# Optimization experiments

Hardware: AMD Instinct MI355X
Metric: run time of the kernel (lower is better)

The kernel has to match this reference:

```python
import jax, jax.numpy as jnp
import numpy as np

N = 50000
E = 800000
NEG_SLOPE = 0.2
BN_EPS = 1e-5


def _gat_conv(x, src, dst, W, a_src, a_dst, bias, heads, out_ch, concat):
    # Linear projection per head: [N, heads, out_ch]
    h = (x @ W).reshape(-1, heads, out_ch)
    # Per-node attention terms alpha_src/alpha_dst: [N, heads]
    al_s = (h * a_src[None]).sum(-1)
    al_d = (h * a_dst[None]).sum(-1)
    # Edge logits with LeakyReLU: [E, heads]
    logits = jax.nn.leaky_relu(al_s[src] + al_d[dst], NEG_SLOPE)
    # Segment (scatter) softmax over edges grouped by destination node
    m = jax.ops.segment_max(logits, dst, num_segments=N)
    e = jnp.exp(logits - m[dst])
    s = jax.ops.segment_sum(e, dst, num_segments=N)
    alpha = e / (s[dst] + 1e-16)                      # [E, heads]
    # Weighted message aggregation: scatter-add to destinations
    msg = h[src] * alpha[:, :, None]                  # [E, heads, out_ch]
    out = jax.ops.segment_sum(msg, dst, num_segments=N)  # [N, heads, out_ch]
    out = out.reshape(-1, heads * out_ch) if concat else out.mean(axis=1)
    return out + bias


def _bn_eval(x, gamma, beta, mean, var):
    return (x - mean) * jax.lax.rsqrt(var + BN_EPS) * gamma + beta


def setup_inputs() -> dict:
    key = jax.random.key(0)
    ks = jax.random.split(key, 12)
    in_ch, hid, heads, out_cls = 128, 64, 2, 40
    return {
        "x": jax.random.normal(ks[0], (N, in_ch), jnp.float32),
        "edge_index": jax.random.randint(ks[1], (2, E), 0, N, jnp.int32),
        "W1": jax.random.normal(ks[2], (in_ch, heads * hid), jnp.float32) * 0.1,
        "a1_src": jax.random.normal(ks[3], (heads, hid), jnp.float32) * 0.1,
        "a1_dst": jax.random.normal(ks[4], (heads, hid), jnp.float32) * 0.1,
        "b1": jnp.zeros((heads * hid,), jnp.float32),
        "bn1_gamma": jnp.ones((heads * hid,), jnp.float32),
        "bn1_beta": jnp.zeros((heads * hid,), jnp.float32),
        "bn1_mean": jax.random.normal(ks[5], (heads * hid,), jnp.float32) * 0.1,
        "bn1_var": jax.random.uniform(ks[6], (heads * hid,), jnp.float32, 0.5, 1.5),
        "W2": jax.random.normal(ks[7], (heads * hid, out_cls), jnp.float32) * 0.1,
        "a2_src": jax.random.normal(ks[8], (1, out_cls), jnp.float32) * 0.1,
        "a2_dst": jax.random.normal(ks[9], (1, out_cls), jnp.float32) * 0.1,
        "b2": jnp.zeros((out_cls,), jnp.float32),
    }


def reference(x, edge_index, W1, a1_src, a1_dst, b1, bn1_gamma, bn1_beta,
              bn1_mean, bn1_var, W2, a2_src, a2_dst, b2):
    # add self loops
    loops = jnp.arange(N, dtype=edge_index.dtype)
    src = jnp.concatenate([edge_index[0], loops])
    dst = jnp.concatenate([edge_index[1], loops])
    # layer 1: GATConv(heads=2, concat) -> BN(eval) -> ReLU (dropout is eval no-op)
    h = _gat_conv(x, src, dst, W1, a1_src, a1_dst, b1, heads=2, out_ch=64, concat=True)
    h = jax.nn.relu(_bn_eval(h, bn1_gamma, bn1_beta, bn1_mean, bn1_var))
    # output layer: GATConv(heads=1, concat=False)
    out = _gat_conv(h, src, dst, W2, a2_src, a2_dst, b2, heads=1, out_ch=40, concat=False)
    return jax.nn.log_softmax(out, axis=1)
```

## Files before the change

kernel.cpp:

```cpp
#include <hip/hip_runtime.h>
#include <hip/hip_bf16.h>

#define NEG_SLOPE 0.2f
#define BN_EPS 1e-5f

#define NBLK 256
#define COARSE_SHIFT 9
#define COARSE_NPB 512

__device__ __forceinline__ float wred_sum(float v) {
    #pragma unroll
    for (int m = 32; m > 0; m >>= 1) v += __shfl_xor(v, m);
    return v;
}
__device__ __forceinline__ float wred_max(float v) {
    #pragma unroll
    for (int m = 32; m > 0; m >>= 1) v = fmaxf(v, __shfl_xor(v, m));
    return v;
}
__device__ __forceinline__ int wred_isum(int v) {
    #pragma unroll
    for (int m = 32; m > 0; m >>= 1) v += __shfl_xor(v, m);
    return v;
}
__device__ __forceinline__ float xor16_sum(float v) {
    #pragma unroll
    for (int m = 1; m < 16; m <<= 1) v += __shfl_xor(v, m);
    return v;
}

__device__ __forceinline__ unsigned pack_bf16(float a, float b) {
    __hip_bfloat162 t;
    t.x = __float2bfloat16(a);
    t.y = __float2bfloat16(b);
    return *(unsigned*)&t;
}
__device__ __forceinline__ float2 unpack_bf16(unsigned u) {
    __hip_bfloat162 t = *(__hip_bfloat162*)&u;
    return {__bfloat162float(t.x), __bfloat162float(t.y)};
}

__device__ __forceinline__ unsigned enc_ord(float f) {
    unsigned u = __float_as_uint(f);
    return (u & 0x80000000u) ? ~u : (u | 0x80000000u);
}
__device__ __forceinline__ float dec_ord(unsigned e) {
    unsigned u = (e & 0x80000000u) ? (e ^ 0x80000000u) : ~e;
    return __uint_as_float(u);
}

__global__ __launch_bounds__(256) void part_hist(const int* __restrict__ ei, int E, int Et,
                                                 int chunk, int* __restrict__ hist, int nCoarse) {
    __shared__ int h[128];
    int b = blockIdx.x, t = threadIdx.x;
    if (t < 128) h[t] = 0;
    __syncthreads();
    int beg = b * chunk, end = min(beg + chunk, Et);
    for (int idx = beg + t; idx < end; idx += 256) {
        int d = (idx < E) ? ei[E + idx] : (idx - E);
        atomicAdd(&h[d >> COARSE_SHIFT], 1);
    }
    __syncthreads();
    if (t < nCoarse) hist[t * NBLK + b] = h[t];
}

__global__ __launch_bounds__(1024) void csr_mid(int* __restrict__ hist,
                                                int* __restrict__ cbase, int nCoarse) {
    __shared__ int ctot_s[128];
    __shared__ int scn[128];
    __shared__ int cb_s[129];
    int t = threadIdx.x;
    int wv = t >> 6, ln = t & 63;
    if (t < 128) ctot_s[t] = 0;
    __syncthreads();
    for (int c = wv; c < nCoarse; c += 16) {
        int idx = c * NBLK + 4 * ln;
        int4 v = *(int4*)&hist[idx];
        int s = wred_isum(v.x + v.y + v.z + v.w);
        if (ln == 0) ctot_s[c] = s;
    }
    __syncthreads();
    int v0 = 0;
    if (t < 128) { v0 = ctot_s[t]; scn[t] = v0; }
    __syncthreads();
    for (int off = 1; off < 128; off <<= 1) {
        int u = (t >= off && t < 128) ? scn[t - off] : 0;
        __syncthreads();
        if (t < 128) scn[t] += u;
        __syncthreads();
    }
    if (t < 128) cb_s[t] = scn[t] - v0;
    if (t == 127) cb_s[128] = scn[127];
    __syncthreads();
    if (t <= nCoarse) cbase[t] = cb_s[t];
    for (int c = wv; c < nCoarse; c += 16) {
        int base = cb_s[c];
        int idx = c * NBLK + 4 * ln;
        int4 v = *(int4*)&hist[idx];
        int sl = v.x + v.y + v.z + v.w;
        int inc = sl;
        #pragma unroll
        for (int off = 1; off < 64; off <<= 1) {
            int u = __shfl_up(inc, off);
            if (ln >= off) inc += u;
        }
        int exc = inc - sl + base;
        int4 o;
        o.x = exc;
        o.y = exc + v.x;
        o.z = exc + v.x + v.y;
        o.w = exc + v.x + v.y + v.z;
        *(int4*)&hist[idx] = o;
    }
}

__global__ __launch_bounds__(256) void part_scatter(const int* __restrict__ ei, int E, int Et,
                                                    int chunk, const int* __restrict__ hist,
                                                    unsigned* __restrict__ staged, int nCoarse) {
    __shared__ int cur[128];
    int b = blockIdx.x, t = threadIdx.x;
    if (t < nCoarse) cur[t] = hist[t * NBLK + b];
    __syncthreads();
    int beg = b * chunk, end = min(beg + chunk, Et);
    for (int idx = beg + t; idx < end; idx += 256) {
        int s, d;
        if (idx < E) { s = ei[idx]; d = ei[E + idx]; }
        else         { s = idx - E; d = idx - E; }
        int c = d >> COARSE_SHIFT;
        int pos = atomicAdd(&cur[c], 1);
        staged[pos] = ((unsigned)s << COARSE_SHIFT) | (unsigned)(d & (COARSE_NPB - 1));
    }
}

__global__ __launch_bounds__(512) void fine_place(const unsigned* __restrict__ staged,
                                                  const int* __restrict__ cbase,
                                                  int* __restrict__ offs,
                                                  int* __restrict__ csr, int Nn, int nCoarse) {
    __shared__ int hcnt[COARSE_NPB];
    __shared__ int scn[COARSE_NPB];
    int b = blockIdx.x, t = threadIdx.x;
    int node0 = b << COARSE_SHIFT;
    int nloc = min(COARSE_NPB, Nn - node0);
    hcnt[t] = 0;
    __syncthreads();
    int ebeg = cbase[b], eend = cbase[b + 1];
    for (int p = ebeg + t; p < eend; p += 512) {
        atomicAdd(&hcnt[staged[p] & (COARSE_NPB - 1)], 1);
    }
    __syncthreads();
    int val = hcnt[t];
    scn[t] = val;
    __syncthreads();
    for (int off = 1; off < COARSE_NPB; off <<= 1) {
        int u = (t >= off) ? scn[t - off] : 0;
        __syncthreads();
        scn[t] += u;
        __syncthreads();
    }
    int exc = ebeg + scn[t] - val;
    if (t < nloc) offs[node0 + t] = exc;
    if (b == nCoarse - 1 && t == 0) offs[Nn] = eend;
    hcnt[t] = exc;
    __syncthreads();
    for (int p = ebeg + t; p < eend; p += 512) {
        unsigned v = staged[p];
        int pos = atomicAdd(&hcnt[v & (COARSE_NPB - 1)], 1);
        csr[pos] = (int)(v >> COARSE_SHIFT);
    }
}

__global__ __launch_bounds__(256) void gemm1_tiled(const float* __restrict__ x,
                                                   const float* __restrict__ W,
                                                   const float* __restrict__ a1s,
                                                   const float* __restrict__ a1d,
                                                   unsigned* __restrict__ h1b,
                                                   float* __restrict__ als,
                                                   float* __restrict__ ald, int Nn) {
    __shared__ float Ast[32][132];
    __shared__ float Bs[32][132];
    int t  = threadIdx.x;
    int tx = t & 15;
    int ty = t >> 4;
    int br = blockIdx.x * 128;

    float acc[8][8];
    #pragma unroll
    for (int i = 0; i < 8; ++i)
        #pragma unroll
        for (int j = 0; j < 8; ++j) acc[i][j] = 0.f;

    int k4   = t & 7;
    int rowA = t >> 3;

    for (int k0 = 0; k0 < 128; k0 += 32) {
        #pragma unroll
        for (int i = 0; i < 4; ++i) {
            int r  = rowA + 32 * i;
            int gr = min(br + r, Nn - 1);
            float4 v = *(const float4*)(x + (size_t)gr * 128 + k0 + 4 * k4);
            Ast[4 * k4 + 0][r] = v.x; Ast[4 * k4 + 1][r] = v.y;
            Ast[4 * k4 + 2][r] = v.z; Ast[4 * k4 + 3][r] = v.w;
        }
        #pragma unroll
        for (int i = 0; i < 4; ++i) {
            int f  = t + 256 * i;
            int kk = f >> 5, c4 = f & 31;
            *(float4*)&Bs[kk][4 * c4] = *(const float4*)(W + (size_t)(k0 + kk) * 128 + 4 * c4);
        }
        __syncthreads();
        #pragma unroll 8
        for (int kk = 0; kk < 32; ++kk) {
            float4 a0 = *(const float4*)&Ast[kk][8 * ty];
            float4 a1 = *(const float4*)&Ast[kk][8 * ty + 4];
            float4 b0 = *(const float4*)&Bs[kk][8 * tx];
            float4 b1 = *(const float4*)&Bs[kk][8 * tx + 4];
            float av[8] = {a0.x, a0.y, a0.z, a0.w, a1.x, a1.y, a1.z, a1.w};
            float bv[8] = {b0.x, b0.y, b0.z, b0.w, b1.x, b1.y, b1.z, b1.w};
            #pragma unroll
            for (int i = 0; i < 8; ++i)
                #pragma unroll
                for (int j = 0; j < 8; ++j) acc[i][j] += av[i] * bv[j];
        }
        __syncthreads();
    }

    float a_s[8], a_d[8];
    #pragma unroll
    for (int j = 0; j < 8; ++j) { a_s[j] = a1s[8 * tx + j]; a_d[j] = a1d[8 * tx + j]; }
    bool h0 = (tx < 8);

    #pragma unroll
    for (int i = 0; i < 8; ++i) {
        int r = br + 8 * ty + i;
        if (r < Nn) {
            uint4 pk;
            pk.x = pack_bf16(acc[i][0], acc[i][1]);
            pk.y = pack_bf16(acc[i][2], acc[i][3]);
            pk.z = pack_bf16(acc[i][4], acc[i][5]);
            pk.w = pack_bf16(acc[i][6], acc[i][7]);
            *(uint4*)(h1b + (size_t)r * 64 + 4 * tx) = pk;
        }
        float ps = 0.f, pd = 0.f;
        #pragma unroll
        for (int j = 0; j < 8; ++j) { ps += acc[i][j] * a_s[j]; pd += acc[i][j] * a_d[j]; }
        float s0 = xor16_sum(h0 ? ps : 0.f);
        float s1 = xor16_sum(h0 ? 0.f : ps);
        float d0 = xor16_sum(h0 ? pd : 0.f);
        float d1 = xor16_sum(h0 ? 0.f : pd);
        if (tx == 0 && r < Nn) {
            als[r * 2] = s0; als[r * 2 + 1] = s1;
            ald[r * 2] = d0; ald[r * 2 + 1] = d1;
        }
    }
}

template <int H>
__global__ __launch_bounds__(256) void almax_kernel(const float* __restrict__ als,
                                                    unsigned* __restrict__ gmax, int off, int Nn,
                                                    const float* __restrict__ b1,
                                                    const float* __restrict__ g1,
                                                    const float* __restrict__ be1,
                                                    const float* __restrict__ mn1,
                                                    const float* __restrict__ vr1,
                                                    float* __restrict__ bnscale,
                                                    float* __restrict__ bnshift) {
    __shared__ float red[4][H];
    int t = threadIdx.x;
    if (bnscale && blockIdx.x == 0 && t < 128) {
        float sc = rsqrtf(vr1[t] + BN_EPS) * g1[t];
        bnscale[t] = sc;
        bnshift[t] = be1[t] + (b1[t] - mn1[t]) * sc;
    }
    float m[H];
    #pragma unroll
    for (int h = 0; h < H; ++h) m[h] = -1e30f;
    for (int n = blockIdx.x * 256 + t; n < Nn; n += gridDim.x * 256) {
        #pragma unroll
        for (int h = 0; h < H; ++h) m[h] = fmaxf(m[h], als[n * H + h]);
    }
    #pragma unroll
    for (int h = 0; h < H; ++h) m[h] = wred_max(m[h]);
    int wid = t >> 6;
    if ((t & 63) == 0) {
        #pragma unroll
        for (int h = 0; h < H; ++h) red[wid][h] = m[h];
    }
    __syncthreads();
    if (t == 0) {
        #pragma unroll
        for (int h = 0; h < H; ++h) {
            float mm = fmaxf(fmaxf(red[0][h], red[1][h]), fmaxf(red[2][h], red[3][h]));
            atomicMax(&gmax[off + h], enc_ord(mm));
        }
    }
}

__global__ __launch_bounds__(256) void softagg1_kernel(const int* __restrict__ offs, const int* __restrict__ csr,
                            const unsigned* __restrict__ h1b,
                            const float* __restrict__ als, const float* __restrict__ ald,
                            const unsigned* __restrict__ gmax,
                            const float* __restrict__ bnscale, const float* __restrict__ bnshift,
                            unsigned* __restrict__ hbnb, int Nn) {
    __shared__ int   sh_s[4][64];
    __shared__ float sh_e0[4][64];
    __shared__ float sh_e1[4][64];
    int wid = threadIdx.x >> 6, lane = threadIdx.x & 63;
    int n = blockIdx.x * 4 + wid;
    if (n >= Nn) return;
    int b = offs[n], e = offs[n + 1];
    float2 aldn = *(const float2*)(ald + n * 2);
    float bd0 = dec_ord(gmax[0]) + aldn.x; bd0 = (bd0 > 0.f) ? bd0 : NEG_SLOPE * bd0;
    float bd1 = dec_ord(gmax[1]) + aldn.y; bd1 = (bd1 > 0.f) ? bd1 : NEG_SLOPE * bd1;

    int eslot = lane >> 3;
    int l8    = lane & 7;
    float acc[16];
    #pragma unroll
    for (int j = 0; j < 16; ++j) acc[j] = 0.f;
    float den0 = 0.f, den1 = 0.f;

    for (int base = b; base < e; base += 64) {
        int cnt = min(64, e - base);
        int   s1 = 0;
        float e0r = 0.f, e1r = 0.f;
        if (lane < cnt) {
            s1 = csr[base + lane];
            float2 as = *(const float2*)(als + (size_t)s1 * 2);
            float l0 = as.x + aldn.x; l0 = (l0 > 0.f) ? l0 : NEG_SLOPE * l0;
            float l1 = as.y + aldn.y; l1 = (l1 > 0.f) ? l1 : NEG_SLOPE * l1;
            e0r = __expf(l0 - bd0);
            e1r = __expf(l1 - bd1);
            den0 += e0r; den1 += e1r;
        }
        sh_s[wid][lane]  = s1;
        sh_e0[wid][lane] = e0r;
        sh_e1[wid][lane] = e1r;
        int i = eslot;
        for (; i + 8 < cnt; i += 16) {
            int   sA  = sh_s[wid][i];
            int   sB  = sh_s[wid][i + 8];
            float e0A = sh_e0[wid][i],  e1A = sh_e1[wid][i];
            float e0B = sh_e0[wid][i + 8], e1B = sh_e1[wid][i + 8];
            const uint4* pA = (const uint4*)(h1b + (size_t)sA * 64 + 4 * l8);
            const uint4* pB = (const uint4*)(h1b + (size_t)sB * 64 + 4 * l8);
            uint4 vaA = pA[0];
            uint4 vbA = pA[8];
            uint4 vaB = pB[0];
            uint4 vbB = pB[8];
            float2 f;
            f = unpack_bf16(vaA.x); acc[0]  += f.x * e0A; acc[1]  += f.y * e0A;
            f = unpack_bf16(vaA.y); acc[2]  += f.x * e0A; acc[3]  += f.y * e0A;
            f = unpack_bf16(vaA.z); acc[4]  += f.x * e0A; acc[5]  += f.y * e0A;
            f = unpack_bf16(vaA.w); acc[6]  += f.x * e0A; acc[7]  += f.y * e0A;
            f = unpack_bf16(vbA.x); acc[8]  += f.x * e1A; acc[9]  += f.y * e1A;
            f = unpack_bf16(vbA.y); acc[10] += f.x * e1A; acc[11] += f.y * e1A;
            f = unpack_bf16(vbA.z); acc[12] += f.x * e1A; acc[13] += f.y * e1A;
            f = unpack_bf16(vbA.w); acc[14] += f.x * e1A; acc[15] += f.y * e1A;
            f = unpack_bf16(vaB.x); acc[0]  += f.x * e0B; acc[1]  += f.y * e0B;
            f = unpack_bf16(vaB.y); acc[2]  += f.x * e0B; acc[3]  += f.y * e0B;
            f = unpack_bf16(vaB.z); acc[4]  += f.x * e0B; acc[5]  += f.y * e0B;
            f = unpack_bf16(vaB.w); acc[6]  += f.x * e0B; acc[7]  += f.y * e0B;
            f = unpack_bf16(vbB.x); acc[8]  += f.x * e1B; acc[9]  += f.y * e1B;
            f = unpack_bf16(vbB.y); acc[10] += f.x * e1B; acc[11] += f.y * e1B;
            f = unpack_bf16(vbB.z); acc[12] += f.x * e1B; acc[13] += f.y * e1B;
            f = unpack_bf16(vbB.w); acc[14] += f.x * e1B; acc[15] += f.y * e1B;
        }
        if (i < cnt) {
            int   s  = sh_s[wid][i];
            float e0 = sh_e0[wid][i], e1 = sh_e1[wid][i];
            const uint4* pR = (const uint4*)(h1b + (size_t)s * 64 + 4 * l8);
            uint4 va = pR[0];
            uint4 vb = pR[8];
            float2 f;
            f = unpack_bf16(va.x); acc[0]  += f.x * e0; acc[1]  += f.y * e0;
            f = unpack_bf16(va.y); acc[2]  += f.x * e0; acc[3]  += f.y * e0;
            f = unpack_bf16(va.z); acc[4]  += f.x * e0; acc[5]  += f.y * e0;
            f = unpack_bf16(va.w); acc[6]  += f.x * e0; acc[7]  += f.y * e0;
            f = unpack_bf16(vb.x); acc[8]  += f.x * e1; acc[9]  += f.y * e1;
            f = unpack_bf16(vb.y); acc[10] += f.x * e1; acc[11] += f.y * e1;
            f = unpack_bf16(vb.z); acc[12] += f.x * e1; acc[13] += f.y * e1;
            f = unpack_bf16(vb.w); acc[14] += f.x * e1; acc[15] += f.y * e1;
        }
    }
    #pragma unroll
    for (int j = 0; j < 16; ++j) {
        acc[j] += __shfl_xor(acc[j], 8);
        acc[j] += __shfl_xor(acc[j], 16);
        acc[j] += __shfl_xor(acc[j], 32);
    }
    den0 = wred_sum(den0);
    den1 = wred_sum(den1);
    if (eslot == 0) {
        float inv0 = 1.f / (den0 + 1e-16f);
        float inv1 = 1.f / (den1 + 1e-16f);
        int c0 = 8 * l8, c1 = 64 + 8 * l8;
        float4 sa = *(const float4*)(bnscale + c0), sb = *(const float4*)(bnscale + c0 + 4);
        float4 ha = *(const float4*)(bnshift + c0), hb = *(const float4*)(bnshift + c0 + 4);
        float o0 = fmaxf(acc[0] * inv0 * sa.x + ha.x, 0.f);
        float o1 = fmaxf(acc[1] * inv0 * sa.y + ha.y, 0.f);
        float o2 = fmaxf(acc[2] * inv0 * sa.z + ha.z, 0.f);
        float o3 = fmaxf(acc[3] * inv0 * sa.w + ha.w, 0.f);
        float o4 = fmaxf(acc[4] * inv0 * sb.x + hb.x, 0.f);
        float o5 = fmaxf(acc[5] * inv0 * sb.y + hb.y, 0.f);
        float o6 = fmaxf(acc[6] * inv0 * sb.z + hb.z, 0.f);
        float o7 = fmaxf(acc[7] * inv0 * sb.w + hb.w, 0.f);
        uint4 pk0 = {pack_bf16(o0, o1), pack_bf16(o2, o3), pack_bf16(o4, o5), pack_bf16(o6, o7)};
        *(uint4*)(hbnb + (size_t)n * 64 + 4 * l8) = pk0;
        float4 sc = *(const float4*)(bnscale + c1), sd = *(const float4*)(bnscale + c1 + 4);
        float4 hc = *(const float4*)(bnshift + c1), hd = *(const float4*)(bnshift + c1 + 4);
        float p0 = fmaxf(acc[8]  * inv1 * sc.x + hc.x, 0.f);
        float p1 = fmaxf(acc[9]  * inv1 * sc.y + hc.y, 0.f);
        float p2 = fmaxf(acc[10] * inv1 * sc.z + hc.z, 0.f);
        float p3 = fmaxf(acc[11] * inv1 * sc.w + hc.w, 0.f);
        float p4 = fmaxf(acc[12] * inv1 * sd.x + hd.x, 0.f);
        float p5 = fmaxf(acc[13] * inv1 * sd.y + hd.y, 0.f);
        float p6 = fmaxf(acc[14] * inv1 * sd.z + hd.z, 0.f);
        float p7 = fmaxf(acc[15] * inv1 * sd.w + hd.w, 0.f);
        uint4 pk1 = {pack_bf16(p0, p1), pack_bf16(p2, p3), pack_bf16(p4, p5), pack_bf16(p6, p7)};
        *(uint4*)(hbnb + (size_t)n * 64 + 32 + 4 * l8) = pk1;
    }
}

__global__ __launch_bounds__(256) void gemm2_tiled(const unsigned* __restrict__ hbnb,
                                                   const float* __restrict__ W2,
                                                   const float* __restrict__ a2s,
                                                   const float* __restrict__ a2d,
                                                   unsigned* __restrict__ h2b,
                                                   float* __restrict__ als, float* __restrict__ ald,
                                                   int Nn) {
    __shared__ float Ast[32][132];
    __shared__ float Bs[32][68];
    int t  = threadIdx.x;
    int tx = t & 15;
    int ty = t >> 4;
    int br = blockIdx.x * 128;

    float as4[4], ad4[4];
    #pragma unroll
    for (int j = 0; j < 4; ++j) {
        int c = 4 * tx + j;
        as4[j] = (c < 40) ? a2s[c] : 0.f;
        ad4[j] = (c < 40) ? a2d[c] : 0.f;
    }

    float acc[8][4];
    #pragma unroll
    for (int i = 0; i < 8; ++i)
        #pragma unroll
        for (int j = 0; j < 4; ++j) acc[i][j] = 0.f;

    int k4   = t & 7;
    int rowA = t >> 3;

    for (int k0 = 0; k0 < 128; k0 += 32) {
        #pragma unroll
        for (int i = 0; i < 4; ++i) {
            int r  = rowA + 32 * i;
            int gr = min(br + r, Nn - 1);
            uint2 v2 = *(const uint2*)(hbnb + (size_t)gr * 64 + (k0 >> 1) + 2 * k4);
            float2 f0 = unpack_bf16(v2.x), f1 = unpack_bf16(v2.y);
            Ast[4 * k4 + 0][r] = f0.x; Ast[4 * k4 + 1][r] = f0.y;
            Ast[4 * k4 + 2][r] = f1.x; Ast[4 * k4 + 3][r] = f1.y;
        }
        #pragma unroll
        for (int i = 0; i < 2; ++i) {
            int f  = t + 256 * i;
            int kk = f >> 4, c4 = f & 15;
            float4 v = {0.f, 0.f, 0.f, 0.f};
            if (c4 < 10) v = *(const float4*)(W2 + (size_t)(k0 + kk) * 40 + 4 * c4);
            *(float4*)&Bs[kk][4 * c4] = v;
        }
        __syncthreads();
        #pragma unroll 8
        for (int kk = 0; kk < 32; ++kk) {
            float4 a0 = *(const float4*)&Ast[kk][8 * ty];
            float4 a1 = *(const float4*)&Ast[kk][8 * ty + 4];
            float4 b0 = *(const float4*)&Bs[kk][4 * tx];
            float av[8] = {a0.x, a0.y, a0.z, a0.w, a1.x, a1.y, a1.z, a1.w};
            #pragma unroll
            for (int i = 0; i < 8; ++i) {
                acc[i][0] += av[i] * b0.x; acc[i][1] += av[i] * b0.y;
                acc[i][2] += av[i] * b0.z; acc[i][3] += av[i] * b0.w;
            }
        }
        __syncthreads();
    }

    #pragma unroll
    for (int i = 0; i < 8; ++i) {
        int r = br + 8 * ty + i;
        if (r < Nn) {
            uint2 pk = {pack_bf16(acc[i][0], acc[i][1]), pack_bf16(acc[i][2], acc[i][3])};
            *(uint2*)(h2b + (size_t)r * 32 + 2 * tx) = pk;
        }
        float ps = acc[i][0] * as4[0] + acc[i][1] * as4[1] + acc[i][2] * as4[2] + acc[i][3] * as4[3];
        float pd = acc[i][0] * ad4[0] + acc[i][1] * ad4[1] + acc[i][2] * ad4[2] + acc[i][3] * ad4[3];
        float sS = xor16_sum(ps);
        float sD = xor16_sum(pd);
        if (tx == 0 && r < Nn) { als[r] = sS; ald[r] = sD; }
    }
}

__global__ __launch_bounds__(256) void softagg2_kernel(const int* __restrict__ offs, const int* __restrict__ csr,
                            const unsigned* __restrict__ h2b,
                            const float* __restrict__ als, const float* __restrict__ ald,
                            const unsigned* __restrict__ gmax,
                            const float* __restrict__ b2,
                            float* __restrict__ out, int Nn) {
    __shared__ int   sh_s[4][64];
    __shared__ float sh_ev[4][64];
    int wid = threadIdx.x >> 6, lane = threadIdx.x & 63;
    int n = blockIdx.x * 4 + wid;
    if (n >= Nn) return;
    int b = offs[n], e = offs[n + 1];
    float aldn = ald[n];
    float bound = dec_ord(gmax[2]) + aldn;
    bound = (bound > 0.f) ? bound : NEG_SLOPE * bound;

    int eslot = lane >> 3;
    int l8    = lane & 7;
    float acc[8];
    #pragma unroll
    for (int j = 0; j < 8; ++j) acc[j] = 0.f;
    float den = 0.f;

    for (int base = b; base < e; base += 64) {
        int cnt = min(64, e - base);
        int   s1 = 0;
        float evr = 0.f;
        if (lane < cnt) {
            s1 = csr[base + lane];
            float l = als[s1] + aldn;
            l = (l > 0.f) ? l : NEG_SLOPE * l;
            evr = __expf(l - bound);
            den += evr;
        }
        sh_s[wid][lane]  = s1;
        sh_ev[wid][lane] = evr;
        int i = eslot;
        for (; i + 8 < cnt; i += 16) {
            int   sA  = sh_s[wid][i];
            int   sB  = sh_s[wid][i + 8];
            float evA = sh_ev[wid][i];
            float evB = sh_ev[wid][i + 8];
            uint4 vA = *(const uint4*)(h2b + (size_t)sA * 32 + 4 * l8);
            uint4 vB = *(const uint4*)(h2b + (size_t)sB * 32 + 4 * l8);
            float2 f;
            f = unpack_bf16(vA.x); acc[0] += f.x * evA; acc[1] += f.y * evA;
            f = unpack_bf16(vA.y); acc[2] += f.x * evA; acc[3] += f.y * evA;
            f = unpack_bf16(vA.z); acc[4] += f.x * evA; acc[5] += f.y * evA;
            f = unpack_bf16(vA.w); acc[6] += f.x * evA; acc[7] += f.y * evA;
            f = unpack_bf16(vB.x); acc[0] += f.x * evB; acc[1] += f.y * evB;
            f = unpack_bf16(vB.y); acc[2] += f.x * evB; acc[3] += f.y * evB;
            f = unpack_bf16(vB.z); acc[4] += f.x * evB; acc[5] += f.y * evB;
            f = unpack_bf16(vB.w); acc[6] += f.x * evB; acc[7] += f.y * evB;
        }
        if (i < cnt) {
            int   s  = sh_s[wid][i];
            float ev = sh_ev[wid][i];
            uint4 v = *(const uint4*)(h2b + (size_t)s * 32 + 4 * l8);
            float2 f;
            f = unpack_bf16(v.x); acc[0] += f.x * ev; acc[1] += f.y * ev;
            f = unpack_bf16(v.y); acc[2] += f.x * ev; acc[3] += f.y * ev;
            f = unpack_bf16(v.z); acc[4] += f.x * ev; acc[5] += f.y * ev;
            f = unpack_bf16(v.w); acc[6] += f.x * ev; acc[7] += f.y * ev;
        }
    }
    #pragma unroll
    for (int j = 0; j < 8; ++j) {
        acc[j] += __shfl_xor(acc[j], 8);
        acc[j] += __shfl_xor(acc[j], 16);
        acc[j] += __shfl_xor(acc[j], 32);
    }
    den = wred_sum(den);
    float inv = 1.f / (den + 1e-16f);
    bool valid = (eslot == 0) && (l8 < 5);
    float vv[8];
    float lmax = -1e30f;
    if (valid) {
        int c = 8 * l8;
        #pragma unroll
        for (int j = 0; j < 8; ++j) {
            vv[j] = acc[j] * inv + b2[c + j];
            lmax = fmaxf(lmax, vv[j]);
        }
    }
    float m = wred_max(lmax);
    float es = 0.f;
    if (valid) {
        #pragma unroll
        for (int j = 0; j < 8; ++j) es += __expf(vv[j] - m);
    }
    float ssum = wred_sum(es);
    float lse = m + logf(ssum);
    if (valid) {
        float4 oa = {vv[0] - lse, vv[1] - lse, vv[2] - lse, vv[3] - lse};
        float4 ob = {vv[4] - lse, vv[5] - lse, vv[6] - lse, vv[7] - lse};
        *(float4*)(out + (size_t)n * 40 + 8 * l8)     = oa;
        *(float4*)(out + (size_t)n * 40 + 8 * l8 + 4) = ob;
    }
}

extern "C" void kernel_launch(void* const* d_in, const int* in_sizes, int n_in,
                              void* d_out, int out_size, void* d_ws, size_t ws_size,
                              hipStream_t stream) {
    const float* x    = (const float*)d_in[0];
    const int*   ei   = (const int*)d_in[1];
    const float* W1   = (const float*)d_in[2];
    const float* a1s  = (const float*)d_in[3];
    const float* a1d  = (const float*)d_in[4];
    const float* b1   = (const float*)d_in[5];
    const float* g1   = (const float*)d_in[6];
    const float* be1  = (const float*)d_in[7];
    const float* mn1  = (const float*)d_in[8];
    const float* vr1  = (const float*)d_in[9];
    const float* W2   = (const float*)d_in[10];
    const float* a2s  = (const float*)d_in[11];
    const float* a2d  = (const float*)d_in[12];
    const float* b2   = (const float*)d_in[13];
    float* out = (float*)d_out;

    const int N  = in_sizes[0] / 128;
    const int E  = in_sizes[1] / 2;
    const int Et = E + N;
    const int nCoarse = (N + COARSE_NPB - 1) >> COARSE_SHIFT;
    const int chunk   = (Et + NBLK - 1) / NBLK;

    char* p = (char*)d_ws;
    auto alloc = [&](size_t bytes) -> void* {
        void* r = (void*)p;
        p += (bytes + 255) & ~(size_t)255;
        return r;
    };
    int*      hist   = (int*)alloc((size_t)nCoarse * NBLK * 4);
    int*      cbase  = (int*)alloc((size_t)(nCoarse + 1) * 4);
    int*      offs   = (int*)alloc((size_t)(N + 1) * 4);
    unsigned* staged = (unsigned*)alloc((size_t)Et * 4);
    int*      csr    = (int*)alloc((size_t)Et * 4);
    unsigned* h1b    = (unsigned*)alloc((size_t)N * 64 * 4);
    float*    al1sv  = (float*)alloc((size_t)N * 2 * 4);
    float*    al1dv  = (float*)alloc((size_t)N * 2 * 4);
    unsigned* hbnb   = (unsigned*)alloc((size_t)N * 64 * 4);
    unsigned* h2b    = (unsigned*)alloc((size_t)N * 32 * 4);
    float*    al2sv  = (float*)alloc((size_t)N * 4);
    float*    al2dv  = (float*)alloc((size_t)N * 4);
    unsigned* gmax   = (unsigned*)alloc(4 * 4);
    float*    bnscale= (float*)alloc(128 * 4);
    float*    bnshift= (float*)alloc(128 * 4);
    (void)ws_size;

    hipMemsetAsync(gmax, 0, 16, stream);

    part_hist<<<NBLK, 256, 0, stream>>>(ei, E, Et, chunk, hist, nCoarse);
    csr_mid<<<1, 1024, 0, stream>>>(hist, cbase, nCoarse);
    part_scatter<<<NBLK, 256, 0, stream>>>(ei, E, Et, chunk, hist, staged, nCoarse);
    fine_place<<<nCoarse, 512, 0, stream>>>(staged, cbase, offs, csr, N, nCoarse);

    gemm1_tiled<<<(N + 127) / 128, 256, 0, stream>>>(x, W1, a1s, a1d, h1b, al1sv, al1dv, N);
    almax_kernel<2><<<64, 256, 0, stream>>>(al1sv, gmax, 0, N, b1, g1, be1, mn1, vr1, bnscale, bnshift);
    softagg1_kernel<<<(N + 3) / 4, 256, 0, stream>>>(offs, csr, h1b, al1sv, al1dv, gmax,
                                                     bnscale, bnshift, hbnb, N);

    gemm2_tiled<<<(N + 127) / 128, 256, 0, stream>>>(hbnb, W2, a2s, a2d, h2b, al2sv, al2dv, N);
    almax_kernel<1><<<64, 256, 0, stream>>>(al2sv, gmax, 2, N, nullptr, nullptr, nullptr, nullptr,
                                            nullptr, nullptr, nullptr);
    softagg2_kernel<<<(N + 3) / 4, 256, 0, stream>>>(offs, csr, h2b, al2sv, al2dv, gmax, b2, out, N);
}
```

Before: 264.9 us.

## Map multiple destination nodes per wavefront and compact layer-2 feature rows

Both aggregation kernels now assign a sub-group of lanes (16 for layer 1, 8 for layer 2) to each destination node instead of a whole 64-lane wavefront. This removes the cross-slot shuffle reductions and the idle lanes caused by the low average degree (about 17). The layer-2 bf16 feature buffer is shrunk from a 32-word row stride to 20 words, which cuts gather bytes. In exchange each lane walks edges serially, so latency for high-degree nodes grows, and there is less memory-level parallelism per node.

Result: faster. 241.3 us (-8.9%).

```diff
diff --git a/kernel.cpp b/kernel.cpp
--- a/kernel.cpp
+++ b/kernel.cpp
@@ -301,30 +301,30 @@
                             const unsigned* __restrict__ gmax,
                             const float* __restrict__ bnscale, const float* __restrict__ bnshift,
                             unsigned* __restrict__ hbnb, int Nn) {
-    __shared__ int   sh_s[4][64];
-    __shared__ float sh_e0[4][64];
-    __shared__ float sh_e1[4][64];
+    __shared__ int   sh_s[4][4][16];
+    __shared__ float sh_e[4][4][2][16];
     int wid = threadIdx.x >> 6, lane = threadIdx.x & 63;
-    int n = blockIdx.x * 4 + wid;
+    int g = lane >> 4;
+    int l = lane & 15;
+    int head = l >> 3;
+    int n = blockIdx.x * 16 + wid * 4 + g;
     if (n >= Nn) return;
     int b = offs[n], e = offs[n + 1];
-    float2 aldn = *(const float2*)(ald + n * 2);
+    float2 aldn = *(const float2*)(ald + (size_t)n * 2);
     float bd0 = dec_ord(gmax[0]) + aldn.x; bd0 = (bd0 > 0.f) ? bd0 : NEG_SLOPE * bd0;
     float bd1 = dec_ord(gmax[1]) + aldn.y; bd1 = (bd1 > 0.f) ? bd1 : NEG_SLOPE * bd1;
 
-    int eslot = lane >> 3;
-    int l8    = lane & 7;
-    float acc[16];
-    #pragma unroll
-    for (int j = 0; j < 16; ++j) acc[j] = 0.f;
+    float acc[8];
+    #pragma unroll
+    for (int j = 0; j < 8; ++j) acc[j] = 0.f;
     float den0 = 0.f, den1 = 0.f;
 
-    for (int base = b; base < e; base += 64) {
-        int cnt = min(64, e - base);
+    for (int base = b; base < e; base += 16) {
+        int cnt = min(16, e - base);
         int   s1 = 0;
         float e0r = 0.f, e1r = 0.f;
-        if (lane < cnt) {
-            s1 = csr[base + lane];
+        if (l < cnt) {
+            s1 = csr[base + l];
             float2 as = *(const float2*)(als + (size_t)s1 * 2);
             float l0 = as.x + aldn.x; l0 = (l0 > 0.f) ? l0 : NEG_SLOPE * l0;
             float l1 = as.y + aldn.y; l1 = (l1 > 0.f) ? l1 : NEG_SLOPE * l1;
@@ -332,93 +332,57 @@
             e1r = __expf(l1 - bd1);
             den0 += e0r; den1 += e1r;
         }
-        sh_s[wid][lane]  = s1;
-        sh_e0[wid][lane] = e0r;
-        sh_e1[wid][lane] = e1r;
-        int i = eslot;
-        for (; i + 8 < cnt; i += 16) {
-            int   sA  = sh_s[wid][i];
-            int   sB  = sh_s[wid][i + 8];
-            float e0A = sh_e0[wid][i],  e1A = sh_e1[wid][i];
-            float e0B = sh_e0[wid][i + 8], e1B = sh_e1[wid][i + 8];
-            const uint4* pA = (const uint4*)(h1b + (size_t)sA * 64 + 4 * l8);
-            const uint4* pB = (const uint4*)(h1b + (size_t)sB * 64 + 4 * l8);
-            uint4 vaA = pA[0];
-            uint4 vbA = pA[8];
-            uint4 vaB = pB[0];
-            uint4 vbB = pB[8];
+        sh_s[wid][g][l]    = s1;
+        sh_e[wid][g][0][l] = e0r;
+        sh_e[wid][g][1][l] = e1r;
+        int i = 0;
+        for (; i + 1 < cnt; i += 2) {
+            int   sA  = sh_s[wid][g][i];
+            int   sB  = sh_s[wid][g][i + 1];
+            float evA = sh_e[wid][g][head][i];
+            float evB = sh_e[wid][g][head][i + 1];
+            uint4 vA = *(const uint4*)(h1b + (size_t)sA * 64 + 4 * l);
+            uint4 vB = *(const uint4*)(h1b + (size_t)sB * 64 + 4 * l);
             float2 f;
-            f = unpack_bf16(vaA.x); acc[0]  += f.x * e0A; acc[1]  += f.y * e0A;
-            f = unpack_bf16(vaA.y); acc[2]  += f.x * e0A; acc[3]  += f.y * e0A;
-            f = unpack_bf16(vaA.z); acc[4]  += f.x * e0A; acc[5]  += f.y * e0A;
-            f = unpack_bf16(vaA.w); acc[6]  += f.x * e0A; acc[7]  += f.y * e0A;
-            f = unpack_bf16(vbA.x); acc[8]  += f.x * e1A; acc[9]  += f.y * e1A;
-            f = unpack_bf16(vbA.y); acc[10] += f.x * e1A; acc[11] += f.y * e1A;
-            f = unpack_bf16(vbA.z); acc[12] += f.x * e1A; acc[13] += f.y * e1A;
-            f = unpack_bf16(vbA.w); acc[14] += f.x * e1A; acc[15] += f.y * e1A;
-            f = unpack_bf16(vaB.x); acc[0]  += f.x * e0B; acc[1]  += f.y * e0B;
-            f = unpack_bf16(vaB.y); acc[2]  += f.x * e0B; acc[3]  += f.y * e0B;
-            f = unpack_bf16(vaB.z); acc[4]  += f.x * e0B; acc[5]  += f.y * e0B;
-            f = unpack_bf16(vaB.w); acc[6]  += f.x * e0B; acc[7]  += f.y * e0B;
-            f = unpack_bf16(vbB.x); acc[8]  += f.x * e1B; acc[9]  += f.y * e1B;
-            f = unpack_bf16(vbB.y); acc[10] += f.x * e1B; acc[11] += f.y * e1B;
-            f = unpack_bf16(vbB.z); acc[12] += f.x * e1B; acc[13] += f.y * e1B;
-            f = unpack_bf16(vbB.w); acc[14] += f.x * e1B; acc[15] += f.y * e1B;
+            f = unpack_bf16(vA.x); acc[0] += f.x * evA; acc[1] += f.y * evA;
+            f = unpack_bf16(vA.y); acc[2] += f.x * evA; acc[3] += f.y * evA;
+            f = unpack_bf16(vA.z); acc[4] += f.x * evA; acc[5] += f.y * evA;
+            f = unpack_bf16(vA.w); acc[6] += f.x * evA; acc[7] += f.y * evA;
+            f = unpack_bf16(vB.x); acc[0] += f.x * evB; acc[1] += f.y * evB;
+            f = unpack_bf16(vB.y); acc[2] += f.x * evB; acc[3] += f.y * evB;
+            f = unpack_bf16(vB.z); acc[4] += f.x * evB; acc[5] += f.y * evB;
+            f = unpack_bf16(vB.w); acc[6] += f.x * evB; acc[7] += f.y * evB;
         }
         if (i < cnt) {
-            int   s  = sh_s[wid][i];
-            float e0 = sh_e0[wid][i], e1 = sh_e1[wid][i];
-            const uint4* pR = (const uint4*)(h1b + (size_t)s * 64 + 4 * l8);
-            uint4 va = pR[0];
-            uint4 vb = pR[8];
+            int   s  = sh_s[wid][g][i];
+            float ev = sh_e[wid][g][head][i];
+            uint4 v = *(const uint4*)(h1b + (size_t)s * 64 + 4 * l);
             float2 f;
-            f = unpack_bf16(va.x); acc[0]  += f.x * e0; acc[1]  += f.y * e0;
-            f = unpack_bf16(va.y); acc[2]  += f.x * e0; acc[3]  += f.y * e0;
-            f = unpack_bf16(va.z); acc[4]  += f.x * e0; acc[5]  += f.y * e0;
-            f = unpack_bf16(va.w); acc[6]  += f.x * e0; acc[7]  += f.y * e0;
-            f = unpack_bf16(vb.x); acc[8]  += f.x * e1; acc[9]  += f.y * e1;
-            f = unpack_bf16(vb.y); acc[10] += f.x * e1; acc[11] += f.y * e1;
-            f = unpack_bf16(vb.z); acc[12] += f.x * e1; acc[13] += f.y * e1;
-            f = unpack_bf16(vb.w); acc[14] += f.x * e1; acc[15] += f.y * e1;
-        }
-    }
-    #pragma unroll
-    for (int j = 0; j < 16; ++j) {
-        acc[j] += __shfl_xor(acc[j], 8);
-        acc[j] += __shfl_xor(acc[j], 16);
-        acc[j] += __shfl_xor(acc[j], 32);
-    }
-    den0 = wred_sum(den0);
-    den1 = wred_sum(den1);
-    if (eslot == 0) {
-        float inv0 = 1.f / (den0 + 1e-16f);
-        float inv1 = 1.f / (den1 + 1e-16f);
-        int c0 = 8 * l8, c1 = 64 + 8 * l8;
-        float4 sa = *(const float4*)(bnscale + c0), sb = *(const float4*)(bnscale + c0 + 4);
-        float4 ha = *(const float4*)(bnshift + c0), hb = *(const float4*)(bnshift + c0 + 4);
-        float o0 = fmaxf(acc[0] * inv0 * sa.x + ha.x, 0.f);
-        float o1 = fmaxf(acc[1] * inv0 * sa.y + ha.y, 0.f);
-        float o2 = fmaxf(acc[2] * inv0 * sa.z + ha.z, 0.f);
-        float o3 = fmaxf(acc[3] * inv0 * sa.w + ha.w, 0.f);
-        float o4 = fmaxf(acc[4] * inv0 * sb.x + hb.x, 0.f);
-        float o5 = fmaxf(acc[5] * inv0 * sb.y + hb.y, 0.f);
-        float o6 = fmaxf(acc[6] * inv0 * sb.z + hb.z, 0.f);
-        float o7 = fmaxf(acc[7] * inv0 * sb.w + hb.w, 0.f);
-        uint4 pk0 = {pack_bf16(o0, o1), pack_bf16(o2, o3), pack_bf16(o4, o5), pack_bf16(o6, o7)};
-        *(uint4*)(hbnb + (size_t)n * 64 + 4 * l8) = pk0;
-        float4 sc = *(const float4*)(bnscale + c1), sd = *(const float4*)(bnscale + c1 + 4);
-        float4 hc = *(const float4*)(bnshift + c1), hd = *(const float4*)(bnshift + c1 + 4);
-        float p0 = fmaxf(acc[8]  * inv1 * sc.x + hc.x, 0.f);
-        float p1 = fmaxf(acc[9]  * inv1 * sc.y + hc.y, 0.f);
-        float p2 = fmaxf(acc[10] * inv1 * sc.z + hc.z, 0.f);
-        float p3 = fmaxf(acc[11] * inv1 * sc.w + hc.w, 0.f);
-        float p4 = fmaxf(acc[12] * inv1 * sd.x + hd.x, 0.f);
-        float p5 = fmaxf(acc[13] * inv1 * sd.y + hd.y, 0.f);
-        float p6 = fmaxf(acc[14] * inv1 * sd.z + hd.z, 0.f);
-        float p7 = fmaxf(acc[15] * inv1 * sd.w + hd.w, 0.f);
-        uint4 pk1 = {pack_bf16(p0, p1), pack_bf16(p2, p3), pack_bf16(p4, p5), pack_bf16(p6, p7)};
-        *(uint4*)(hbnb + (size_t)n * 64 + 32 + 4 * l8) = pk1;
-    }
+            f = unpack_bf16(v.x); acc[0] += f.x * ev; acc[1] += f.y * ev;
+            f = unpack_bf16(v.y); acc[2] += f.x * ev; acc[3] += f.y * ev;
+            f = unpack_bf16(v.z); acc[4] += f.x * ev; acc[5] += f.y * ev;
+            f = unpack_bf16(v.w); acc[6] += f.x * ev; acc[7] += f.y * ev;
+        }
+    }
+    #pragma unroll
+    for (int m = 1; m < 16; m <<= 1) {
+        den0 += __shfl_xor(den0, m);
+        den1 += __shfl_xor(den1, m);
+    }
+    float inv = 1.f / ((head ? den1 : den0) + 1e-16f);
+    int c = 8 * l;
+    float4 sa = *(const float4*)(bnscale + c), sb = *(const float4*)(bnscale + c + 4);
+    float4 ha = *(const float4*)(bnshift + c), hb = *(const float4*)(bnshift + c + 4);
+    float o0 = fmaxf(acc[0] * inv * sa.x + ha.x, 0.f);
+    float o1 = fmaxf(acc[1] * inv * sa.y + ha.y, 0.f);
+    float o2 = fmaxf(acc[2] * inv * sa.z + ha.z, 0.f);
+    float o3 = fmaxf(acc[3] * inv * sa.w + ha.w, 0.f);
+    float o4 = fmaxf(acc[4] * inv * sb.x + hb.x, 0.f);
+    float o5 = fmaxf(acc[5] * inv * sb.y + hb.y, 0.f);
+    float o6 = fmaxf(acc[6] * inv * sb.z + hb.z, 0.f);
+    float o7 = fmaxf(acc[7] * inv * sb.w + hb.w, 0.f);
+    uint4 pk = {pack_bf16(o0, o1), pack_bf16(o2, o3), pack_bf16(o4, o5), pack_bf16(o6, o7)};
+    *(uint4*)(hbnb + (size_t)n * 64 + 4 * l) = pk;
 }
 
 __global__ __launch_bounds__(256) void gemm2_tiled(const unsigned* __restrict__ hbnb,
@@ -489,9 +453,9 @@
     #pragma unroll
     for (int i = 0; i < 8; ++i) {
         int r = br + 8 * ty + i;
-        if (r < Nn) {
+        if (r < Nn && tx < 10) {
             uint2 pk = {pack_bf16(acc[i][0], acc[i][1]), pack_bf16(acc[i][2], acc[i][3])};
-            *(uint2*)(h2b + (size_t)r * 32 + 2 * tx) = pk;
+            *(uint2*)(h2b + (size_t)r * 20 + 2 * tx) = pk;
         }
         float ps = acc[i][0] * as4[0] + acc[i][1] * as4[1] + acc[i][2] * as4[2] + acc[i][3] * as4[3];
         float pd = acc[i][0] * ad4[0] + acc[i][1] * ad4[1] + acc[i][2] * ad4[2] + acc[i][3] * ad4[3];
@@ -507,97 +471,97 @@
                             const unsigned* __restrict__ gmax,
                             const float* __restrict__ b2,
                             float* __restrict__ out, int Nn) {
-    __shared__ int   sh_s[4][64];
-    __shared__ float sh_ev[4][64];
+    __shared__ int   sh_s[4][8][8];
+    __shared__ float sh_ev[4][8][8];
     int wid = threadIdx.x >> 6, lane = threadIdx.x & 63;
-    int n = blockIdx.x * 4 + wid;
+    int g = lane >> 3;
+    int l = lane & 7;
+    int n = blockIdx.x * 32 + wid * 8 + g;
     if (n >= Nn) return;
     int b = offs[n], e = offs[n + 1];
     float aldn = ald[n];
     float bound = dec_ord(gmax[2]) + aldn;
     bound = (bound > 0.f) ? bound : NEG_SLOPE * bound;
 
-    int eslot = lane >> 3;
-    int l8    = lane & 7;
     float acc[8];
     #pragma unroll
     for (int j = 0; j < 8; ++j) acc[j] = 0.f;
     float den = 0.f;
 
-    for (int base = b; base < e; base += 64) {
-        int cnt = min(64, e - base);
+    for (int base = b; base < e; base += 8) {
+        int cnt = min(8, e - base);
         int   s1 = 0;
         float evr = 0.f;
-        if (lane < cnt) {
-            s1 = csr[base + lane];
-            float l = als[s1] + aldn;
-            l = (l > 0.f) ? l : NEG_SLOPE * l;
-            evr = __expf(l - bound);
+        if (l < cnt) {
+            s1 = csr[base + l];
+            float lv = als[s1] + aldn;
+            lv = (lv > 0.f) ? lv : NEG_SLOPE * lv;
+            evr = __expf(lv - bound);
             den += evr;
         }
-        sh_s[wid][lane]  = s1;
-        sh_ev[wid][lane] = evr;
-        int i = eslot;
-        for (; i + 8 < cnt; i += 16) {
-            int   sA  = sh_s[wid][i];
-            int   sB  = sh_s[wid][i + 8];
-            float evA = sh_ev[wid][i];
-            float evB = sh_ev[wid][i + 8];
-            uint4 vA = *(const uint4*)(h2b + (size_t)sA * 32 + 4 * l8);
-            uint4 vB = *(const uint4*)(h2b + (size_t)sB * 32 + 4 * l8);
-            float2 f;
-            f = unpack_bf16(vA.x); acc[0] += f.x * evA; acc[1] += f.y * evA;
-            f = unpack_bf16(vA.y); acc[2] += f.x * evA; acc[3] += f.y * evA;
-            f = unpack_bf16(vA.z); acc[4] += f.x * evA; acc[5] += f.y * evA;
-            f = unpack_bf16(vA.w); acc[6] += f.x * evA; acc[7] += f.y * evA;
-            f = unpack_bf16(vB.x); acc[0] += f.x * evB; acc[1] += f.y * evB;
-            f = unpack_bf16(vB.y); acc[2] += f.x * evB; acc[3] += f.y * evB;
-            f = unpack_bf16(vB.z); acc[4] += f.x * evB; acc[5] += f.y * evB;
-            f = unpack_bf16(vB.w); acc[6] += f.x * evB; acc[7] += f.y * evB;
-        }
-        if (i < cnt) {
-            int   s  = sh_s[wid][i];
-            float ev = sh_ev[wid][i];
-            uint4 v = *(const uint4*)(h2b + (size_t)s * 32 + 4 * l8);
-            float2 f;
-            f = unpack_bf16(v.x); acc[0] += f.x * ev; acc[1] += f.y * ev;
-            f = unpack_bf16(v.y); acc[2] += f.x * ev; acc[3] += f.y * ev;
-            f = unpack_bf16(v.z); acc[4] += f.x * ev; acc[5] += f.y * ev;
-            f = unpack_bf16(v.w); acc[6] += f.x * ev; acc[7] += f.y * ev;
-        }
-    }
-    #pragma unroll
-    for (int j = 0; j < 8; ++j) {
-        acc[j] += __shfl_xor(acc[j], 8);
-        acc[j] += __shfl_xor(acc[j], 16);
-        acc[j] += __shfl_xor(acc[j], 32);
-    }
-    den = wred_sum(den);
+        sh_s[wid][g][l]  = s1;
+        sh_ev[wid][g][l] = evr;
+        if (l < 5) {
+            int i = 0;
+            for (; i + 1 < cnt; i += 2) {
+                int   sA  = sh_s[wid][g][i];
+                int   sB  = sh_s[wid][g][i + 1];
+                float evA = sh_ev[wid][g][i];
+                float evB = sh_ev[wid][g][i + 1];
+                uint4 vA = *(const uint4*)(h2b + (size_t)sA * 20 + 4 * l);
+                uint4 vB = *(const uint4*)(h2b + (size_t)sB * 20 + 4 * l);
+                float2 f;
+                f = unpack_bf16(vA.x); acc[0] += f.x * evA; acc[1] += f.y * evA;
+                f = unpack_bf16(vA.y); acc[2] += f.x * evA; acc[3] += f.y * evA;
+                f = unpack_bf16(vA.z); acc[4] += f.x * evA; acc[5] += f.y * evA;
+                f = unpack_bf16(vA.w); acc[6] += f.x * evA; acc[7] += f.y * evA;
+                f = unpack_bf16(vB.x); acc[0] += f.x * evB; acc[1] += f.y * evB;
+                f = unpack_bf16(vB.y); acc[2] += f.x * evB; acc[3] += f.y * evB;
+                f = unpack_bf16(vB.z); acc[4] += f.x * evB; acc[5] += f.y * evB;
+                f = unpack_bf16(vB.w); acc[6] += f.x * evB; acc[7] += f.y * evB;
+            }
+            if (i < cnt) {
+                int   s  = sh_s[wid][g][i];
+                float ev = sh_ev[wid][g][i];
+                uint4 v = *(const uint4*)(h2b + (size_t)s * 20 + 4 * l);
+                float2 f;
+                f = unpack_bf16(v.x); acc[0] += f.x * ev; acc[1] += f.y * ev;
+                f = unpack_bf16(v.y); acc[2] += f.x * ev; acc[3] += f.y * ev;
+                f = unpack_bf16(v.z); acc[4] += f.x * ev; acc[5] += f.y * ev;
+                f = unpack_bf16(v.w); acc[6] += f.x * ev; acc[7] += f.y * ev;
+            }
+        }
+    }
+    #pragma unroll
+    for (int m = 1; m < 8; m <<= 1) den += __shfl_xor(den, m);
     float inv = 1.f / (den + 1e-16f);
-    bool valid = (eslot == 0) && (l8 < 5);
+    bool valid = (l < 5);
     float vv[8];
     float lmax = -1e30f;
     if (valid) {
-        int c = 8 * l8;
+        int c = 8 * l;
         #pragma unroll
         for (int j = 0; j < 8; ++j) {
             vv[j] = acc[j] * inv + b2[c + j];
             lmax = fmaxf(lmax, vv[j]);
         }
     }
-    float m = wred_max(lmax);
+    float m = lmax;
+    #pragma unroll
+    for (int mm = 1; mm < 8; mm <<= 1) m = fmaxf(m, __shfl_xor(m, mm));
     float es = 0.f;
     if (valid) {
         #pragma unroll
         for (int j = 0; j < 8; ++j) es += __expf(vv[j] - m);
     }
-    float ssum = wred_sum(es);
-    float lse = m + logf(ssum);
+    #pragma unroll
+    for (int mm = 1; mm < 8; mm <<= 1) es += __shfl_xor(es, mm);
+    float lse = m + logf(es);
     if (valid) {
         float4 oa = {vv[0] - lse, vv[1] - lse, vv[2] - lse, vv[3] - lse};
         float4 ob = {vv[4] - lse, vv[5] - lse, vv[6] - lse, vv[7] - lse};
-        *(float4*)(out + (size_t)n * 40 + 8 * l8)     = oa;
-        *(float4*)(out + (size_t)n * 40 + 8 * l8 + 4) = ob;
+        *(float4*)(out + (size_t)n * 40 + 8 * l)     = oa;
+        *(float4*)(out + (size_t)n * 40 + 8 * l + 4) = ob;
     }
 }
 
@@ -641,7 +605,7 @@
     float*    al1sv  = (float*)alloc((size_t)N * 2 * 4);
     float*    al1dv  = (float*)alloc((size_t)N * 2 * 4);
     unsigned* hbnb   = (unsigned*)alloc((size_t)N * 64 * 4);
-    unsigned* h2b    = (unsigned*)alloc((size_t)N * 32 * 4);
+    unsigned* h2b    = (unsigned*)alloc((size_t)N * 20 * 4);
     float*    al2sv  = (float*)alloc((size_t)N * 4);
     float*    al2dv  = (float*)alloc((size_t)N * 4);
     unsigned* gmax   = (unsigned*)alloc(4 * 4);
@@ -658,11 +622,11 @@
 
     gemm1_tiled<<<(N + 127) / 128, 256, 0, stream>>>(x, W1, a1s, a1d, h1b, al1sv, al1dv, N);
     almax_kernel<2><<<64, 256, 0, stream>>>(al1sv, gmax, 0, N, b1, g1, be1, mn1, vr1, bnscale, bnshift);
-    softagg1_kernel<<<(N + 3) / 4, 256, 0, stream>>>(offs, csr, h1b, al1sv, al1dv, gmax,
-                                                     bnscale, bnshift, hbnb, N);
+    softagg1_kernel<<<(N + 15) / 16, 256, 0, stream>>>(offs, csr, h1b, al1sv, al1dv, gmax,
+                                                       bnscale, bnshift, hbnb, N);
 
     gemm2_tiled<<<(N + 127) / 128, 256, 0, stream>>>(hbnb, W2, a2s, a2d, h2b, al2sv, al2dv, N);
     almax_kernel<1><<<64, 256, 0, stream>>>(al2sv, gmax, 2, N, nullptr, nullptr, nullptr, nullptr,
                                             nullptr, nullptr, nullptr);
-    softagg2_kernel<<<(N + 3) / 4, 256, 0, stream>>>(offs, csr, h2b, al2sv, al2dv, gmax, b2, out, N);
-}
+    softagg2_kernel<<<(N + 31) / 32, 256, 0, stream>>>(offs, csr, h2b, al2sv, al2dv, gmax, b2, out, N);
+}
```
